# Kernel optimization log

Measured on AMD Instinct MI355X. Metric: run time of the kernel, lower is better.

## Reference

```python
import jax, jax.numpy as jnp
import numpy as np

N_TOK, TOKDIM = 2048, 1024
NHEADS, KDIM = 16, 64


def setup_inputs() -> dict:
    key = jax.random.key(0)
    kg, kk, kq = jax.random.split(key, 3)
    g = jax.random.normal(kg, (N_TOK, TOKDIM), dtype=jnp.float32)
    # params use normal(stddev=0.002) init, as in the flax module
    Wk = 0.002 * jax.random.normal(kk, (NHEADS, KDIM, TOKDIM), dtype=jnp.float32)
    Wq = 0.002 * jax.random.normal(kq, (NHEADS, KDIM, TOKDIM), dtype=jnp.float32)
    return {"g": g, "Wk": Wk, "Wq": Wq}


def reference(g, Wk, Wq):
    """manual_grad of the attention energy: returns d(energy)/dg, shape [n, d]."""
    H, Z, D = Wk.shape
    betas = jnp.full((H,), 1.0, dtype=g.dtype) / jnp.sqrt(jnp.asarray(Z, g.dtype))
    K = jnp.einsum('hzd,kd->khz', Wk, g)   # [n,h,z]
    Q = jnp.einsum('hzd,qd->qhz', Wq, g)   # [n,h,z]
    F1 = jnp.einsum('hzd,khz->khd', Wq, K)  # [n,h,d]
    F2 = jnp.einsum('hzd,qhz->qhd', Wk, Q)  # [n,h,d]
    A1 = jnp.einsum('h,khz,qhz->hqk', betas, K, Q)  # [h,q,k] scores
    A2 = jax.nn.softmax(A1, -1)
    T1 = -jnp.einsum('khd,hqk->qd', F1, A2)
    T2 = -jnp.einsum('qhd,hqk->kd', F2, A2)
    return T1 + T2
```

## Files before the change

### kernel.cpp

```cpp
#include <hip/hip_runtime.h>
#include <stdint.h>

#define NT 2048
#define TD 1024
#define NH 16
static constexpr float SCL = 0.18033688011112042f;

typedef __attribute__((ext_vector_type(8))) short bf16x8;
typedef __attribute__((ext_vector_type(4))) float f32x4;
typedef __attribute__((ext_vector_type(16))) float f32x16;
typedef __attribute__((address_space(3))) uint32_t lds_u32;
typedef __attribute__((address_space(1))) uint32_t glb_u32;

__device__ __forceinline__ float bf2f(unsigned short u){
  union { uint32_t u32; float f; } v; v.u32 = ((uint32_t)u) << 16; return v.f;
}
__device__ __forceinline__ unsigned short f2bf(float f){
  union { float f; uint32_t u; } v; v.f = f;
  uint32_t r = v.u + 0x7fffu + ((v.u >> 16) & 1u);
  return (unsigned short)(r >> 16);
}
__device__ __forceinline__ bf16x8 ld8(const unsigned short* base, int row, int kc){
  return *(const bf16x8*)((const char*)base + row*128 + ((kc ^ (row & 7)) << 4));
}
template<int N> __device__ __forceinline__ void wait_vm_lgkm0(){
  if constexpr (N == 0)      asm volatile("s_waitcnt vmcnt(0) lgkmcnt(0)" ::: "memory");
  else if constexpr (N == 4) asm volatile("s_waitcnt vmcnt(4) lgkmcnt(0)" ::: "memory");
  else if constexpr (N == 6) asm volatile("s_waitcnt vmcnt(6) lgkmcnt(0)" ::: "memory");
  __builtin_amdgcn_sched_barrier(0);
}

__global__ __launch_bounds__(256) void prep_kernel(
    const float* __restrict__ g, const float* __restrict__ Wk, const float* __restrict__ Wq,
    unsigned short* __restrict__ gbf, unsigned short* __restrict__ wkq,
    unsigned short* __restrict__ twqk)
{
  int b = blockIdx.x;
  if (b < 1024) {
    int base = b * 2048 + threadIdx.x;
    #pragma unroll
    for (int i = 0; i < 8; i++) { int idx = base + i * 256; gbf[idx] = f2bf(g[idx]); }
  } else if (b < 2048) {
    int base = (b - 1024) * 2048 + threadIdx.x;
    #pragma unroll
    for (int i = 0; i < 8; i++) {
      int idx = base + i * 256;
      float v = (idx < (1 << 20)) ? Wk[idx] : Wq[idx - (1 << 20)];
      wkq[idx] = f2bf(v);
    }
  } else {
    int t = b - 2048;
    int dt = t & 31, jt = t >> 5;
    __shared__ float tile[32][33];
    int tx = threadIdx.x & 31, ty = threadIdx.x >> 5;
    int j0 = jt * 32, d0 = dt * 32;
    const float* src = (j0 < 1024) ? Wq : Wk;
    int jb = (j0 < 1024) ? j0 : (j0 - 1024);
    #pragma unroll
    for (int rr = 0; rr < 4; rr++)
      tile[ty + rr * 8][tx] = src[(size_t)(jb + ty + rr * 8) * 1024 + d0 + tx];
    __syncthreads();
    #pragma unroll
    for (int rr = 0; rr < 4; rr++)
      twqk[(size_t)(d0 + ty + rr * 8) * 2048 + j0 + tx] = f2bf(tile[tx][ty + rr * 8]);
  }
}

__global__ __launch_bounds__(256) void pack_pck(const unsigned short* __restrict__ CKQ,
                                                unsigned short* __restrict__ PCK)
{
  int tile = blockIdx.x;
  int cb = tile >> 6, rb = tile & 63;
  __shared__ unsigned short t[32][72];
  int tid = threadIdx.x;
  int r = tid >> 3, c0 = (tid & 7) * 8;
  const unsigned short* src = CKQ + (size_t)(rb * 32 + r) * 2048 + cb * 64 + c0;
  *(ushort4*)&t[r][c0]     = *(const ushort4*)src;
  *(ushort4*)&t[r][c0 + 4] = *(const ushort4*)(src + 4);
  __syncthreads();
  int kz = tid >> 6, l = tid & 63;
  int zl = kz * 16 + 8 * (l >> 5);
  ushort4 lo = *(ushort4*)&t[l & 31][zl];
  ushort4 hi4 = *(ushort4*)&t[l & 31][zl + 4];
  unsigned short* dst = PCK + ((size_t)(tile * 4 + kz) * 64 + l) * 8;
  *(ushort4*)dst       = lo;
  *(ushort4*)(dst + 4) = hi4;
}

template<bool DIVL>
__global__ __launch_bounds__(256) void pack_pbx(const unsigned short* __restrict__ CKQ,
                                                const float* __restrict__ L,
                                                unsigned short* __restrict__ PBX)
{
  int bid = blockIdx.x;
  int qb = bid & 63, hz = bid >> 6;
  int h = hz >> 1, zb = hz & 1;
  int colbase = (DIVL ? 1024 : 0) + h * 64 + zb * 32;
  __shared__ unsigned short tq[32][36];
  __shared__ float rcpL[32];
  int tid = threadIdx.x;
  int r = tid >> 3, c0 = (tid & 7) * 4;
  *(ushort4*)&tq[r][c0] =
      *(const ushort4*)(CKQ + (size_t)(qb * 32 + r) * 2048 + colbase + c0);
  if (DIVL && tid < 32) rcpL[tid] = 1.0f / L[(size_t)h * NT + qb * 32 + tid];
  __syncthreads();
  if (tid < 128) {
    int ks = tid >> 6, l = tid & 63;
    int zl = l & 31, hi = l >> 5;
    unsigned short ob[8];
    #pragma unroll
    for (int e = 0; e < 8; e++) {
      int ql = 16 * ks + 8 * (e >> 2) + 4 * hi + (e & 3);
      unsigned short v = tq[ql][zl];
      if (DIVL) v = f2bf(bf2f(v) * rcpL[ql]);
      ob[e] = v;
    }
    unsigned short* dst = PBX + ((size_t)(bid * 2 + ks) * 64 + l) * 8;
    *(ushort4*)dst       = *(ushort4*)&ob[0];
    *(ushort4*)(dst + 4) = *(ushort4*)&ob[4];
  }
}

template<int TM, int TN, int EPI, int WPE>
__global__ __launch_bounds__(256, WPE) void btg2_kernel(
    const unsigned short* __restrict__ A, int lda,
    const unsigned short* __restrict__ BT, int ldb,
    int Kdim, void* C0)
{
  constexpr int WM = TM / 2, WN = TN / 2, FM = WM / 16, FN = WN / 16;
  constexpr int AC = TM / 32, BC = TN / 32, LOADS = AC + BC;
  __shared__ __align__(16) unsigned short As[3][TM * 64];
  __shared__ __align__(16) unsigned short Bs[3][TN * 64];
  int tid = threadIdx.x, lane = tid & 63, wave = tid >> 6;
  int wr = wave >> 1, wc = wave & 1, lrow = lane & 15, g = lane >> 4;
  int bm = blockIdx.x * TM, bn = blockIdx.y * TN;

  auto stage = [&](unsigned short* bufA, unsigned short* bufB, int kk) {
    #pragma unroll
    for (int i = 0; i < AC; i++) {
      int c = i * 256 + tid, row = c >> 3, sl = ((c & 7) ^ (row & 7)) << 3;
      __builtin_amdgcn_global_load_lds((glb_u32*)(A + (size_t)(bm + row) * lda + kk + sl),
          (lds_u32*)((char*)bufA + i * 4096 + wave * 1024), 16, 0, 0);
    }
    #pragma unroll
    for (int i = 0; i < BC; i++) {
      int c = i * 256 + tid, row = c >> 3, sl = ((c & 7) ^ (row & 7)) << 3;
      __builtin_amdgcn_global_load_lds((glb_u32*)(BT + (size_t)(bn + row) * ldb + kk + sl),
          (lds_u32*)((char*)bufB + i * 4096 + wave * 1024), 16, 0, 0);
    }
  };

  f32x4 acc[FM][FN] = {};
  int nt = Kdim >> 6;
  stage(As[0], Bs[0], 0);
  stage(As[1], Bs[1], 64);
  wait_vm_lgkm0<LOADS>();
  __builtin_amdgcn_s_barrier();
  int bc = 0;
  for (int t = 0; t < nt; t++) {
    int bp = bc + 2; if (bp >= 3) bp -= 3;
    if (t + 2 < nt) stage(As[bp], Bs[bp], (t + 2) * 64);
    const unsigned short* Ac = As[bc];
    const unsigned short* Bc = Bs[bc];
    #pragma unroll
    for (int k2 = 0; k2 < 2; k2++) {
      bf16x8 a_[FM], b_[FN];
      #pragma unroll
      for (int m = 0; m < FM; m++) a_[m] = ld8(Ac, wr * WM + m * 16 + lrow, k2 * 4 + g);
      #pragma unroll
      for (int n = 0; n < FN; n++) b_[n] = ld8(Bc, wc * WN + n * 16 + lrow, k2 * 4 + g);
      #pragma unroll
      for (int m = 0; m < FM; m++)
        #pragma unroll
        for (int n = 0; n < FN; n++)
          acc[m][n] = __builtin_amdgcn_mfma_f32_16x16x32_bf16(a_[m], b_[n], acc[m][n], 0, 0, 0);
    }
    if (t + 2 < nt) wait_vm_lgkm0<LOADS>(); else wait_vm_lgkm0<0>();
    __builtin_amdgcn_s_barrier();
    bc = (bc == 2) ? 0 : bc + 1;
  }
  #pragma unroll
  for (int m = 0; m < FM; m++) {
    int rb = bm + wr * WM + m * 16 + 4 * g;
    #pragma unroll
    for (int n = 0; n < FN; n++) {
      int cc = bn + wc * WN + n * 16 + lrow;
      f32x4 v = acc[m][n];
      if constexpr (EPI == 0) {
        unsigned short* Cp = (unsigned short*)C0;
        #pragma unroll
        for (int j = 0; j < 4; j++) Cp[(size_t)(rb + j) * 2048 + cc] = f2bf(v[j]);
      } else {
        float* Cf = (float*)C0;
        #pragma unroll
        for (int j = 0; j < 4; j++) Cf[(size_t)(rb + j) * 1024 + cc] = -v[j];
      }
    }
  }
}

template<bool DIV>
__global__ __launch_bounds__(256, 2) void fused_kernel(
    const unsigned short* __restrict__ PCK,
    const unsigned short* __restrict__ PBX,
    unsigned short* __restrict__ C,
    float* __restrict__ Lg)
{
  __shared__ __align__(16) float Red[2][64][68];
  __shared__ float L_lds[64];
  int tid = threadIdx.x, l = tid & 63, w = tid >> 6;
  int zr = l & 31, hi = l >> 5;
  int lin = blockIdx.x;
  int wgid = (lin & 7) * 64 + (lin >> 3);
  int h = wgid >> 5, pB = wgid & 31, p0 = pB * 64;
  int cbA = DIV ? h : 16 + h;
  int cbB = DIV ? 16 + h : h;
  const bf16x8* PCKf = (const bf16x8*)PCK;
  const bf16x8* PBXf = (const bf16x8*)PBX;

  bf16x8 bs[2][4];
  #pragma unroll
  for (int ps = 0; ps < 2; ps++)
    #pragma unroll
    for (int kz = 0; kz < 4; kz++)
      bs[ps][kz] = PCKf[((size_t)(cbB * 64 + pB * 2 + ps) * 4 + kz) * 64 + l];

  auto load = [&](bf16x8 (&a_)[4], bf16x8 (&pb_)[2][2], int rb){
    #pragma unroll
    for (int kz = 0; kz < 4; kz++)
      a_[kz] = PCKf[((size_t)(cbA * 64 + rb) * 4 + kz) * 64 + l];
    #pragma unroll
    for (int zb = 0; zb < 2; zb++)
      #pragma unroll
      for (int ks = 0; ks < 2; ks++)
        pb_[zb][ks] = PBXf[((size_t)((h * 2 + zb) * 64 + rb) * 2 + ks) * 64 + l];
  };

  f32x16 acc_pv[2][2] = {};
  float lsum[2] = {0.f, 0.f};
  bf16x8 a_c[4], pb_c[2][2];
  load(a_c, pb_c, w * 16);

  for (int t = 0; t < 16; t++) {
    bf16x8 a_n[4], pb_n[2][2];
    if (t + 1 < 16) load(a_n, pb_n, w * 16 + t + 1);
    f32x16 acc_s[2] = {};
    #pragma unroll
    for (int kz = 0; kz < 4; kz++) {
      acc_s[0] = __builtin_amdgcn_mfma_f32_32x32x16_bf16(a_c[kz], bs[0][kz], acc_s[0], 0, 0, 0);
      acc_s[1] = __builtin_amdgcn_mfma_f32_32x32x16_bf16(a_c[kz], bs[1][kz], acc_s[1], 0, 0, 0);
    }
    union { bf16x8 v; uint32_t u[4]; } pu[2][2];
    #pragma unroll
    for (int ps = 0; ps < 2; ps++) {
      float ev[16];
      #pragma unroll
      for (int r = 0; r < 16; r++) ev[r] = exp2f(acc_s[ps][r] * SCL);
      if (DIV) {
        #pragma unroll
        for (int r = 0; r < 16; r++) lsum[ps] += ev[r];
      }
      #pragma unroll
      for (int ks = 0; ks < 2; ks++)
        #pragma unroll
        for (int i = 0; i < 4; i++)
          asm("v_cvt_pk_bf16_f32 %0, %1, %2"
              : "=v"(pu[ps][ks].u[i]) : "v"(ev[8 * ks + 2 * i]), "v"(ev[8 * ks + 2 * i + 1]));
    }
    #pragma unroll
    for (int zb = 0; zb < 2; zb++)
      #pragma unroll
      for (int ks = 0; ks < 2; ks++) {
        acc_pv[0][zb] = __builtin_amdgcn_mfma_f32_32x32x16_bf16(pu[0][ks].v, pb_c[zb][ks], acc_pv[0][zb], 0, 0, 0);
        acc_pv[1][zb] = __builtin_amdgcn_mfma_f32_32x32x16_bf16(pu[1][ks].v, pb_c[zb][ks], acc_pv[1][zb], 0, 0, 0);
      }
    #pragma unroll
    for (int kz = 0; kz < 4; kz++) a_c[kz] = a_n[kz];
    #pragma unroll
    for (int zb = 0; zb < 2; zb++)
      #pragma unroll
      for (int ks = 0; ks < 2; ks++) pb_c[zb][ks] = pb_n[zb][ks];
  }

  if (w >= 2) {
    #pragma unroll
    for (int ps = 0; ps < 2; ps++)
      #pragma unroll
      for (int zb = 0; zb < 2; zb++) {
        int z = zb * 32 + zr;
        #pragma unroll
        for (int u = 0; u < 4; u++) {
          int p = ps * 32 + 8 * u + 4 * hi;
          f32x4 q;
          q[0] = acc_pv[ps][zb][4 * u];     q[1] = acc_pv[ps][zb][4 * u + 1];
          q[2] = acc_pv[ps][zb][4 * u + 2]; q[3] = acc_pv[ps][zb][4 * u + 3];
          *(f32x4*)&Red[w - 2][z][p] = q;
        }
      }
  }
  if (DIV && tid < 64) L_lds[tid] = 0.f;
  __syncthreads();
  if (w < 2) {
    #pragma unroll
    for (int ps = 0; ps < 2; ps++)
      #pragma unroll
      for (int zb = 0; zb < 2; zb++) {
        int z = zb * 32 + zr;
        #pragma unroll
        for (int u = 0; u < 4; u++) {
          int p = ps * 32 + 8 * u + 4 * hi;
          float* slot = &Red[w][z][p];
          f32x4 q = *(f32x4*)slot;
          q[0] += acc_pv[ps][zb][4 * u];     q[1] += acc_pv[ps][zb][4 * u + 1];
          q[2] += acc_pv[ps][zb][4 * u + 2]; q[3] += acc_pv[ps][zb][4 * u + 3];
          *(f32x4*)slot = q;
        }
      }
  }
  if (DIV) {
    #pragma unroll
    for (int ps = 0; ps < 2; ps++) {
      float s = lsum[ps];
      s += __shfl_xor(s, 32);
      if (hi == 0) atomicAdd(&L_lds[ps * 32 + zr], s);
    }
  }
  __syncthreads();
  if (DIV && tid < 64) Lg[(size_t)h * NT + p0 + tid] = L_lds[tid];
  int p = tid >> 2, z16 = (tid & 3) * 16;
  float inv = DIV ? 1.0f / L_lds[p] : 1.0f;
  int cbase = DIV ? h * 64 : TD + h * 64;
  unsigned short ob[16];
  #pragma unroll
  for (int i = 0; i < 16; i++) {
    int z = z16 + i;
    float x = Red[0][z][p] + Red[1][z][p];
    ob[i] = f2bf(x * inv);
  }
  unsigned short* dst = C + (size_t)(p0 + p) * 2048 + cbase + z16;
  *(ushort4*)dst        = *(ushort4*)&ob[0];
  *(ushort4*)(dst + 4)  = *(ushort4*)&ob[4];
  *(ushort4*)(dst + 8)  = *(ushort4*)&ob[8];
  *(ushort4*)(dst + 12) = *(ushort4*)&ob[12];
}

extern "C" void kernel_launch(void* const* d_in, const int* in_sizes, int n_in,
                              void* d_out, int out_size, void* d_ws, size_t ws_size,
                              hipStream_t stream)
{
  (void)in_sizes; (void)n_in; (void)out_size; (void)ws_size;
  const float* g  = (const float*)d_in[0];
  const float* Wk = (const float*)d_in[1];
  const float* Wq = (const float*)d_in[2];

  char* ws = (char*)d_ws;
  size_t off = 0;
  auto alloc = [&](size_t b) -> char* {
    char* p = ws + off; off += (b + 255) & ~((size_t)255); return p;
  };
  unsigned short* gbf  = (unsigned short*)alloc((size_t)NT * TD * 2);
  unsigned short* wkq  = (unsigned short*)alloc((size_t)2 * TD * TD * 2);
  unsigned short* twqk = (unsigned short*)alloc((size_t)TD * 2048 * 2);
  unsigned short* CKQ  = (unsigned short*)alloc((size_t)NT * 2048 * 2);
  unsigned short* PCK  = (unsigned short*)alloc((size_t)NT * 2048 * 2);
  unsigned short* PBT  = (unsigned short*)alloc((size_t)TD * NT * 2);
  unsigned short* QSTP = (unsigned short*)alloc((size_t)TD * NT * 2);
  unsigned short* CB12 = (unsigned short*)alloc((size_t)NT * 2048 * 2);
  float*          Lbuf = (float*)alloc((size_t)NH * NT * 4);

  prep_kernel<<<dim3(4096), dim3(256), 0, stream>>>(g, Wk, Wq, gbf, wkq, twqk);

  btg2_kernel<128, 64, 0, 2><<<dim3(16, 32), dim3(256), 0, stream>>>(
      gbf, TD, wkq, TD, TD, (void*)CKQ);

  pack_pck<<<dim3(2048), dim3(256), 0, stream>>>(CKQ, PCK);
  pack_pbx<false><<<dim3(2048), dim3(256), 0, stream>>>(CKQ, nullptr, PBT);

  fused_kernel<true><<<dim3(512), dim3(256), 0, stream>>>(PCK, PBT, CB12, Lbuf);

  pack_pbx<true><<<dim3(2048), dim3(256), 0, stream>>>(CKQ, Lbuf, QSTP);

  fused_kernel<false><<<dim3(512), dim3(256), 0, stream>>>(PCK, QSTP, CB12, nullptr);

  btg2_kernel<64, 64, 4, 3><<<dim3(32, 16), dim3(256), 0, stream>>>(
      CB12, 2048, twqk, 2048, 2048, d_out);
}
```

Before: 111.8 us.

## Split-K final GEMM with combine kernel and software-pipeline fused attention loop

The final output GEMM (K=2048) is split into two K halves across blockIdx.z. Each half writes fp32 partials to a workspace, and a new combine kernel sums and negates them. This doubles the grid from 512 to 1024 blocks to fill more CUs, at the cost of an extra 16 MB of partial traffic and an extra launch. The fused attention kernel loop is also restructured so the score MFMA and exp for the next tile are issued after the PV MFMA of the current tile, letting the two overlap.

Result: slower. 122.4 us (+9.4%).

```diff
diff --git a/kernel.cpp b/kernel.cpp
--- a/kernel.cpp
+++ b/kernel.cpp
@@ -134,18 +134,19 @@
   int tid = threadIdx.x, lane = tid & 63, wave = tid >> 6;
   int wr = wave >> 1, wc = wave & 1, lrow = lane & 15, g = lane >> 4;
   int bm = blockIdx.x * TM, bn = blockIdx.y * TN;
+  int kb = blockIdx.z * Kdim;
 
   auto stage = [&](unsigned short* bufA, unsigned short* bufB, int kk) {
     #pragma unroll
     for (int i = 0; i < AC; i++) {
       int c = i * 256 + tid, row = c >> 3, sl = ((c & 7) ^ (row & 7)) << 3;
-      __builtin_amdgcn_global_load_lds((glb_u32*)(A + (size_t)(bm + row) * lda + kk + sl),
+      __builtin_amdgcn_global_load_lds((glb_u32*)(A + (size_t)(bm + row) * lda + kb + kk + sl),
           (lds_u32*)((char*)bufA + i * 4096 + wave * 1024), 16, 0, 0);
     }
     #pragma unroll
     for (int i = 0; i < BC; i++) {
       int c = i * 256 + tid, row = c >> 3, sl = ((c & 7) ^ (row & 7)) << 3;
-      __builtin_amdgcn_global_load_lds((glb_u32*)(BT + (size_t)(bn + row) * ldb + kk + sl),
+      __builtin_amdgcn_global_load_lds((glb_u32*)(BT + (size_t)(bn + row) * ldb + kb + kk + sl),
           (lds_u32*)((char*)bufB + i * 4096 + wave * 1024), 16, 0, 0);
     }
   };
@@ -191,12 +192,24 @@
         #pragma unroll
         for (int j = 0; j < 4; j++) Cp[(size_t)(rb + j) * 2048 + cc] = f2bf(v[j]);
       } else {
-        float* Cf = (float*)C0;
-        #pragma unroll
-        for (int j = 0; j < 4; j++) Cf[(size_t)(rb + j) * 1024 + cc] = -v[j];
+        float* Cf = (float*)C0 + (size_t)blockIdx.z * ((size_t)NT * 1024);
+        #pragma unroll
+        for (int j = 0; j < 4; j++) Cf[(size_t)(rb + j) * 1024 + cc] = v[j];
       }
     }
   }
+}
+
+__global__ __launch_bounds__(256) void comb_kernel(const float* __restrict__ P,
+                                                   float* __restrict__ out)
+{
+  int i = (blockIdx.x * 256 + threadIdx.x) * 4;
+  f32x4 a = *(const f32x4*)&P[i];
+  f32x4 b = *(const f32x4*)&P[i + ((size_t)NT * 1024)];
+  f32x4 r;
+  #pragma unroll
+  for (int j = 0; j < 4; j++) r[j] = -(a[j] + b[j]);
+  *(f32x4*)&out[i] = r;
 }
 
 template<bool DIV>
@@ -225,10 +238,12 @@
     for (int kz = 0; kz < 4; kz++)
       bs[ps][kz] = PCKf[((size_t)(cbB * 64 + pB * 2 + ps) * 4 + kz) * 64 + l];
 
-  auto load = [&](bf16x8 (&a_)[4], bf16x8 (&pb_)[2][2], int rb){
+  auto loadA = [&](bf16x8 (&a_)[4], int rb){
     #pragma unroll
     for (int kz = 0; kz < 4; kz++)
       a_[kz] = PCKf[((size_t)(cbA * 64 + rb) * 4 + kz) * 64 + l];
+  };
+  auto loadB = [&](bf16x8 (&pb_)[2][2], int rb){
     #pragma unroll
     for (int zb = 0; zb < 2; zb++)
       #pragma unroll
@@ -236,21 +251,14 @@
         pb_[zb][ks] = PBXf[((size_t)((h * 2 + zb) * 64 + rb) * 2 + ks) * 64 + l];
   };
 
-  f32x16 acc_pv[2][2] = {};
-  float lsum[2] = {0.f, 0.f};
-  bf16x8 a_c[4], pb_c[2][2];
-  load(a_c, pb_c, w * 16);
-
-  for (int t = 0; t < 16; t++) {
-    bf16x8 a_n[4], pb_n[2][2];
-    if (t + 1 < 16) load(a_n, pb_n, w * 16 + t + 1);
+  union upk { bf16x8 v; uint32_t u[4]; };
+  auto do_S = [&](upk (&pu)[2][2], const bf16x8 (&a_)[4], float (&ls)[2]){
     f32x16 acc_s[2] = {};
     #pragma unroll
     for (int kz = 0; kz < 4; kz++) {
-      acc_s[0] = __builtin_amdgcn_mfma_f32_32x32x16_bf16(a_c[kz], bs[0][kz], acc_s[0], 0, 0, 0);
-      acc_s[1] = __builtin_amdgcn_mfma_f32_32x32x16_bf16(a_c[kz], bs[1][kz], acc_s[1], 0, 0, 0);
-    }
-    union { bf16x8 v; uint32_t u[4]; } pu[2][2];
+      acc_s[0] = __builtin_amdgcn_mfma_f32_32x32x16_bf16(a_[kz], bs[0][kz], acc_s[0], 0, 0, 0);
+      acc_s[1] = __builtin_amdgcn_mfma_f32_32x32x16_bf16(a_[kz], bs[1][kz], acc_s[1], 0, 0, 0);
+    }
     #pragma unroll
     for (int ps = 0; ps < 2; ps++) {
       float ev[16];
@@ -258,7 +266,7 @@
       for (int r = 0; r < 16; r++) ev[r] = exp2f(acc_s[ps][r] * SCL);
       if (DIV) {
         #pragma unroll
-        for (int r = 0; r < 16; r++) lsum[ps] += ev[r];
+        for (int r = 0; r < 16; r++) ls[ps] += ev[r];
       }
       #pragma unroll
       for (int ks = 0; ks < 2; ks++)
@@ -267,20 +275,41 @@
           asm("v_cvt_pk_bf16_f32 %0, %1, %2"
               : "=v"(pu[ps][ks].u[i]) : "v"(ev[8 * ks + 2 * i]), "v"(ev[8 * ks + 2 * i + 1]));
     }
+  };
+
+  f32x16 acc_pv[2][2] = {};
+  float lsum[2] = {0.f, 0.f};
+  bf16x8 a_[4], pb_[2][2];
+  upk pu[2][2];
+
+  loadA(a_, w * 16);
+  loadB(pb_, w * 16);
+  do_S(pu, a_, lsum);
+
+  for (int t = 1; t < 16; t++) {
+    bf16x8 an[4]; bf16x8 pbn[2][2];
+    loadA(an, w * 16 + t);
+    loadB(pbn, w * 16 + t);
     #pragma unroll
     for (int zb = 0; zb < 2; zb++)
       #pragma unroll
       for (int ks = 0; ks < 2; ks++) {
-        acc_pv[0][zb] = __builtin_amdgcn_mfma_f32_32x32x16_bf16(pu[0][ks].v, pb_c[zb][ks], acc_pv[0][zb], 0, 0, 0);
-        acc_pv[1][zb] = __builtin_amdgcn_mfma_f32_32x32x16_bf16(pu[1][ks].v, pb_c[zb][ks], acc_pv[1][zb], 0, 0, 0);
+        acc_pv[0][zb] = __builtin_amdgcn_mfma_f32_32x32x16_bf16(pu[0][ks].v, pb_[zb][ks], acc_pv[0][zb], 0, 0, 0);
+        acc_pv[1][zb] = __builtin_amdgcn_mfma_f32_32x32x16_bf16(pu[1][ks].v, pb_[zb][ks], acc_pv[1][zb], 0, 0, 0);
       }
-    #pragma unroll
-    for (int kz = 0; kz < 4; kz++) a_c[kz] = a_n[kz];
+    do_S(pu, an, lsum);
     #pragma unroll
     for (int zb = 0; zb < 2; zb++)
       #pragma unroll
-      for (int ks = 0; ks < 2; ks++) pb_c[zb][ks] = pb_n[zb][ks];
-  }
+      for (int ks = 0; ks < 2; ks++) pb_[zb][ks] = pbn[zb][ks];
+  }
+  #pragma unroll
+  for (int zb = 0; zb < 2; zb++)
+    #pragma unroll
+    for (int ks = 0; ks < 2; ks++) {
+      acc_pv[0][zb] = __builtin_amdgcn_mfma_f32_32x32x16_bf16(pu[0][ks].v, pb_[zb][ks], acc_pv[0][zb], 0, 0, 0);
+      acc_pv[1][zb] = __builtin_amdgcn_mfma_f32_32x32x16_bf16(pu[1][ks].v, pb_[zb][ks], acc_pv[1][zb], 0, 0, 0);
+    }
 
   if (w >= 2) {
     #pragma unroll
@@ -366,11 +395,12 @@
   unsigned short* PBT  = (unsigned short*)alloc((size_t)TD * NT * 2);
   unsigned short* QSTP = (unsigned short*)alloc((size_t)TD * NT * 2);
   unsigned short* CB12 = (unsigned short*)alloc((size_t)NT * 2048 * 2);
+  float*          PART = (float*)alloc((size_t)2 * NT * 1024 * 4);
   float*          Lbuf = (float*)alloc((size_t)NH * NT * 4);
 
   prep_kernel<<<dim3(4096), dim3(256), 0, stream>>>(g, Wk, Wq, gbf, wkq, twqk);
 
-  btg2_kernel<128, 64, 0, 2><<<dim3(16, 32), dim3(256), 0, stream>>>(
+  btg2_kernel<128, 64, 0, 2><<<dim3(16, 32, 1), dim3(256), 0, stream>>>(
       gbf, TD, wkq, TD, TD, (void*)CKQ);
 
   pack_pck<<<dim3(2048), dim3(256), 0, stream>>>(CKQ, PCK);
@@ -382,6 +412,8 @@
 
   fused_kernel<false><<<dim3(512), dim3(256), 0, stream>>>(PCK, QSTP, CB12, nullptr);
 
-  btg2_kernel<64, 64, 4, 3><<<dim3(32, 16), dim3(256), 0, stream>>>(
-      CB12, 2048, twqk, 2048, 2048, d_out);
-}
+  btg2_kernel<64, 64, 5, 3><<<dim3(32, 16, 2), dim3(256), 0, stream>>>(
+      CB12, 2048, twqk, 2048, 1024, (void*)PART);
+
+  comb_kernel<<<dim3(2048), dim3(256), 0, stream>>>(PART, (float*)d_out);
+}
```
